# Performance work log

Hardware: AMD Instinct MI355X
Metric: run time of the kernel (lower is better)

## Reference

```python
import jax, jax.numpy as jnp
import numpy as np

# --- fixed module hyperparameters (from init_kwargs) ---
B, N, DIM = 1, 1024, 1024
HEADS, KV_HEADS, DH = 16, 4, 64
BS = 32                 # block_size
NUM_SEL = 8             # num_selected_blocks (< num blocks, so min() is NUM_SEL)
MEM = 1                 # num_compressed_mem_kv
W = N // BS             # num compress blocks (seq divisible by block -> no padding paths)
G = HEADS // KV_HEADS   # grouped queries per kv head
CDIM = BS * DH          # compress mlp input dim
HID = CDIM              # compress_mlp_expand_factor = 1.0
EPS = 1e-6


def setup_inputs() -> dict:
    key = jax.random.key(0)
    ks = jax.random.split(key, 12)
    s = 0.02
    f32 = jnp.float32
    return {
        "inp": jax.random.normal(ks[0], (B, N, DIM), f32),
        "g_norm": jnp.ones((DIM,), f32),                                   # RMSNorm weight
        "w_qkv": jax.random.normal(ks[1], (DIM, (HEADS + 2 * KV_HEADS) * DH), f32) * s,
        "mem_kv": jax.random.normal(ks[2], (2, KV_HEADS, MEM, DH), f32) * s,
        "k_pos": jax.random.normal(ks[3], (KV_HEADS, BS, DH), f32) * s,    # intra-block pos
        "v_pos": jax.random.normal(ks[4], (KV_HEADS, BS, DH), f32) * s,
        "k_w1": jax.random.normal(ks[5], (CDIM, HID), f32) * s,
        "k_b1": jnp.zeros((HID,), f32),
        "k_w2": jax.random.normal(ks[6], (HID, DH), f32) * s,
        "k_b2": jnp.zeros((DH,), f32),
        "v_w1": jax.random.normal(ks[7], (CDIM, HID), f32) * s,
        "v_b1": jnp.zeros((HID,), f32),
        "v_w2": jax.random.normal(ks[8], (HID, DH), f32) * s,
        "v_b2": jnp.zeros((DH,), f32),
        "gate_w": jax.random.normal(ks[9], (DIM, 2 * HEADS), f32) * s,
        "gate_b": jnp.full((2 * HEADS,), -2.0, f32),                       # bias init from source
        "w_out": jax.random.normal(ks[10], (HEADS * DH, DIM), f32) * s,
    }


def _rotary(x):
    # interleaved rotary (rotary-embedding-torch default), x: (b, h, n, d)
    n, d = x.shape[-2], x.shape[-1]
    inv_freq = 1.0 / (10000.0 ** (jnp.arange(0, d, 2, dtype=jnp.float32) / d))
    freqs = jnp.arange(n, dtype=jnp.float32)[:, None] * inv_freq            # (n, d/2)
    cos = jnp.repeat(jnp.cos(freqs), 2, axis=-1).astype(x.dtype)
    sin = jnp.repeat(jnp.sin(freqs), 2, axis=-1).astype(x.dtype)
    xr = jnp.stack([-x[..., 1::2], x[..., 0::2]], axis=-1).reshape(x.shape)  # rotate_half
    return x * cos + xr * sin


def reference(inp, g_norm, w_qkv, mem_kv, k_pos, v_pos,
              k_w1, k_b1, k_w2, k_b2, v_w1, v_b1, v_w2, v_b2,
              gate_w, gate_b, w_out):
    scale = DH ** -0.5
    # RMSNorm
    x = inp * jax.lax.rsqrt(jnp.mean(jnp.square(inp), -1, keepdims=True) + EPS) * g_norm
    qkv = x @ w_qkv
    q = qkv[..., : HEADS * DH].reshape(B, N, HEADS, DH).transpose(0, 2, 1, 3)
    k = qkv[..., HEADS * DH : (HEADS + KV_HEADS) * DH].reshape(B, N, KV_HEADS, DH).transpose(0, 2, 1, 3)
    v = qkv[..., (HEADS + KV_HEADS) * DH :].reshape(B, N, KV_HEADS, DH).transpose(0, 2, 1, 3)

    # --- compressed branch: MLP-pool each block of BS keys/values ---
    kpe = k + jnp.tile(k_pos, (1, W, 1))[None]               # (B,KV,N,DH)
    vpe = v + jnp.tile(v_pos, (1, W, 1))[None]
    ck = jax.nn.relu(kpe.reshape(B, KV_HEADS, W, CDIM) @ k_w1 + k_b1) @ k_w2 + k_b2   # (B,KV,W,DH)
    cv = jax.nn.relu(vpe.reshape(B, KV_HEADS, W, CDIM) @ v_w1 + v_b1) @ v_w2 + v_b2
    ck = jnp.concatenate([jnp.broadcast_to(mem_kv[0], (B, KV_HEADS, MEM, DH)), ck], axis=2)
    cv = jnp.concatenate([jnp.broadcast_to(mem_kv[1], (B, KV_HEADS, MEM, DH)), cv], axis=2)

    qg = q.reshape(B, KV_HEADS, G, N, DH)
    csim = jnp.einsum('bhgid,bhjd->bhgij', qg, ck) * scale   # (B,KV,G,N,MEM+W)
    cattn = jax.nn.softmax(csim, axis=-1)
    c_out = jnp.einsum('bhgij,bhjd->bhgid', cattn, cv).reshape(B, HEADS, N, DH)

    # rotary only for the fine branch (applied after compressed attention)
    q = _rotary(q)
    k = _rotary(k)

    # --- block selection from compressed similarities (query heads share) ---
    imp = csim[..., MEM:].mean(axis=2)                       # (B,KV,N,W)
    imp = jnp.pad(imp, ((0, 0), (0, 0), (0, 0), (1, 0)), constant_values=-1000.0)
    imp = jax.nn.softmax(imp, axis=-1)[..., 1:]
    sel_vals, sel_idx = jax.lax.top_k(imp, NUM_SEL)          # (B,KV,N,S)
    fmask = sel_vals > 1e-10

    # always include each query's own block (diagonal block), fully attended
    own = jnp.broadcast_to((jnp.arange(N) // BS)[None, None, :, None], (B, KV_HEADS, N, 1))
    sel_idx = jnp.concatenate([sel_idx, own], axis=-1)       # (B,KV,N,S+1)
    fmask = jnp.concatenate([fmask, jnp.ones(own.shape, bool)], axis=-1)

    # --- gather selected KV blocks per query position (irregular access) ---
    kb = k.reshape(B, KV_HEADS, W, BS, DH)
    vb = v.reshape(B, KV_HEADS, W, BS, DH)
    b_ix = jnp.arange(B)[:, None, None, None]
    h_ix = jnp.arange(KV_HEADS)[None, :, None, None]
    J = (NUM_SEL + 1) * BS
    fk = kb[b_ix, h_ix, sel_idx].reshape(B, KV_HEADS, N, J, DH)
    fv = vb[b_ix, h_ix, sel_idx].reshape(B, KV_HEADS, N, J, DH)
    fmask = jnp.repeat(fmask, BS, axis=-1)                   # (B,KV,N,J)

    fq = q.reshape(B, KV_HEADS, G, N, DH)
    fsim = jnp.einsum('bhgid,bhijd->bhgij', fq, fk) * scale  # (B,KV,G,N,J)
    fsim = jnp.where(fmask[:, :, None], fsim, -jnp.finfo(fsim.dtype).max)
    fattn = jax.nn.softmax(fsim, axis=-1)
    f_out = jnp.einsum('bhgij,bhijd->bhgid', fattn, fv).reshape(B, HEADS, N, DH)

    # --- learned sigmoid gating of the two branches ---
    gates = jax.nn.sigmoid(x @ gate_w + gate_b).reshape(B, N, HEADS, 2).transpose(0, 2, 1, 3)
    out = gates[..., 0:1] * c_out + gates[..., 1:2] * f_out  # (B,H,N,DH)
    out = out.transpose(0, 2, 1, 3).reshape(B, N, HEADS * DH)
    return out @ w_out
```

## Files before the change

### kernel.cpp

```cpp
#include <hip/hip_runtime.h>
#include <math.h>

#define NTOK 1024
#define DDIM 1024
#define HEADS 16
#define KVH 4
#define DH 64
#define BSZ 32
#define NSEL 8
#define WBLK 32
#define GQ 4
#define CDIM 2048
#define HIDN 2048
#define QKVD 1536
#define SCALE 0.125f
#define NEGINF (-__builtin_inff())

typedef unsigned short u16;
typedef u16   u16x8  __attribute__((ext_vector_type(8)));
typedef short short8 __attribute__((ext_vector_type(8)));
typedef float f32x4  __attribute__((ext_vector_type(4)));

__device__ __forceinline__ u16 f2bf(float f) {
    unsigned u = __float_as_uint(f);
    return (u16)((u + 0x7fffu + ((u >> 16) & 1u)) >> 16);
}
__device__ __forceinline__ float bf2f(u16 h) { return __uint_as_float(((unsigned)h) << 16); }

__device__ __forceinline__ void glds16(const void* g, void* l) {
    __builtin_amdgcn_global_load_lds(
        (const __attribute__((address_space(1))) unsigned int*)g,
        (__attribute__((address_space(3))) unsigned int*)l, 16, 0, 0);
}

__device__ __forceinline__ size_t tiled_off(int row, int k, int K) {
    return ((size_t)((row >> 4) * (K >> 5) + (k >> 5)) * 64 +
            ((row & 15) | (((k >> 3) & 3) << 4))) * 8;
}

__global__ void rmsnorm_kernel(const float* __restrict__ inp, const float* __restrict__ g,
                               u16* __restrict__ xhi, u16* __restrict__ xlo) {
    int t = threadIdx.x;
    int half = t >> 7, tid = t & 127;
    int n = blockIdx.x * 2 + half;
    const float4* row = (const float4*)(inp + (size_t)n * DDIM);
    float4 v0 = row[tid * 2], v1 = row[tid * 2 + 1];
    float ss = v0.x*v0.x + v0.y*v0.y + v0.z*v0.z + v0.w*v0.w
             + v1.x*v1.x + v1.y*v1.y + v1.z*v1.z + v1.w*v1.w;
    for (int off = 32; off; off >>= 1) ss += __shfl_down(ss, off);
    __shared__ float red[4];
    if ((t & 63) == 0) red[t >> 6] = ss;
    __syncthreads();
    float tot = red[half * 2] + red[half * 2 + 1];
    float r = 1.f / sqrtf(tot * (1.f / DDIM) + 1e-6f);
    const float4* gp = (const float4*)g;
    float4 g0 = gp[tid * 2], g1 = gp[tid * 2 + 1];
    float o[8] = { v0.x*r*g0.x, v0.y*r*g0.y, v0.z*r*g0.z, v0.w*r*g0.w,
                   v1.x*r*g1.x, v1.y*r*g1.y, v1.z*r*g1.z, v1.w*r*g1.w };
    u16x8 h, l;
#pragma unroll
    for (int i = 0; i < 8; ++i) {
        u16 hh = f2bf(o[i]);
        h[i] = hh;
        l[i] = f2bf(o[i] - bf2f(hh));
    }
    size_t ob = tiled_off(n, tid * 8, DDIM);
    *(u16x8*)&xhi[ob] = h;
    *(u16x8*)&xlo[ob] = l;
}

__global__ void transpose_split(const float* __restrict__ W, u16* __restrict__ Thi,
                                u16* __restrict__ Tlo, int K, int N) {
    __shared__ float tile[64][65];
    int k0 = blockIdx.y * 64, n0 = blockIdx.x * 64;
    int t = threadIdx.x;
    int r = t >> 4, c4 = (t & 15) * 4;
#pragma unroll
    for (int p = 0; p < 4; ++p) {
        float4 v = *(const float4*)&W[(size_t)(k0 + r + p * 16) * N + n0 + c4];
        tile[r + p * 16][c4 + 0] = v.x;
        tile[r + p * 16][c4 + 1] = v.y;
        tile[r + p * 16][c4 + 2] = v.z;
        tile[r + p * 16][c4 + 3] = v.w;
    }
    __syncthreads();
    int n = t >> 2, ks = (t & 3) * 16;
#pragma unroll
    for (int c = 0; c < 2; ++c) {
        u16x8 h, l;
#pragma unroll
        for (int j = 0; j < 8; ++j) {
            float v = tile[ks + c * 8 + j][n];
            u16 hh = f2bf(v);
            h[j] = hh;
            l[j] = f2bf(v - bf2f(hh));
        }
        size_t ob = tiled_off(n0 + n, k0 + ks + c * 8, K);
        *(u16x8*)&Thi[ob] = h;
        if (Tlo) *(u16x8*)&Tlo[ob] = l;
    }
}

__global__ void pad_small_tiled(const float* __restrict__ W, const float* __restrict__ b,
                                u16* __restrict__ Thi, u16* __restrict__ Tlo,
                                float* __restrict__ bias_pad, int K, int Xn, int KLOG) {
    int idx = blockIdx.x * 256 + threadIdx.x;
    int k = (idx & ((K >> 3) - 1)) * 8;
    int n = idx >> (KLOG - 3);
    if (n >= 128) return;
    u16x8 h, l;
#pragma unroll
    for (int j = 0; j < 8; ++j) {
        float v = (n < Xn) ? W[(size_t)(k + j) * Xn + n] : 0.f;
        u16 hh = f2bf(v);
        h[j] = hh;
        l[j] = f2bf(v - bf2f(hh));
    }
    size_t ob = tiled_off(n, k, K);
    *(u16x8*)&Thi[ob] = h;
    *(u16x8*)&Tlo[ob] = l;
    if (k == 0) bias_pad[n] = (n < Xn) ? b[n] : 0.f;
}

template<int SPLIT, int ACT, int FINAL>
__global__ __launch_bounds__(256, 1)
void gemm_tiled(const u16* __restrict__ Ahi0, const u16* __restrict__ Alo0,
                const u16* __restrict__ Bhi0, const u16* __restrict__ Blo0,
                const float* __restrict__ bias0, float* __restrict__ C0,
                const u16* __restrict__ Ahi1, const u16* __restrict__ Alo1,
                const u16* __restrict__ Bhi1, const u16* __restrict__ Blo1,
                const float* __restrict__ bias1, float* __restrict__ C1,
                int M, int N, int K, int S) {
    int batch = blockIdx.z / S;
    int s = blockIdx.z - batch * S;
    const u16* Ahi = batch ? Ahi1 : Ahi0;
    const u16* Alo = batch ? Alo1 : Alo0;
    const u16* Bhi = batch ? Bhi1 : Bhi0;
    const u16* Blo = batch ? Blo1 : Blo0;
    const float* bias = batch ? bias1 : bias0;
    float* C = batch ? C1 : C0;

    constexpr int PARTS = (SPLIT == 3) ? 2 : 1;
    __shared__ u16 smA[2 * PARTS * 8 * 512];
    __shared__ u16 smB[2 * PARTS * 8 * 512];

    int tid = threadIdx.x;
    int w = tid >> 6, L = tid & 63;
    int m15 = L & 15, q = L >> 4;
    int KT = K >> 5;
    int rowTile = blockIdx.y * 8, colTile = blockIdx.x * 8;
    int NIT = (K / S) >> 5;
    int kb0 = s * NIT;
    int aw = w & 1, bw = w >> 1;

    f32x4 acc[4][4];
#pragma unroll
    for (int i = 0; i < 4; ++i)
#pragma unroll
        for (int j = 0; j < 4; ++j) acc[i][j] = (f32x4){0.f, 0.f, 0.f, 0.f};

    auto stage = [&](int buf, int kb) {
#pragma unroll
        for (int rl = 0; rl < 2; ++rl) {
            int rb = 2 * w + rl;
            glds16(Ahi + ((size_t)(rowTile + rb) * KT + kb) * 512 + (size_t)L * 8,
                   &smA[((buf * PARTS + 0) * 8 + rb) * 512]);
            glds16(Bhi + ((size_t)(colTile + rb) * KT + kb) * 512 + (size_t)L * 8,
                   &smB[((buf * PARTS + 0) * 8 + rb) * 512]);
            if constexpr (SPLIT == 3) {
                glds16(Alo + ((size_t)(rowTile + rb) * KT + kb) * 512 + (size_t)L * 8,
                       &smA[((buf * PARTS + 1) * 8 + rb) * 512]);
                glds16(Blo + ((size_t)(colTile + rb) * KT + kb) * 512 + (size_t)L * 8,
                       &smB[((buf * PARTS + 1) * 8 + rb) * 512]);
            }
        }
    };

    stage(0, kb0);
    for (int it = 0; it < NIT; ++it) {
        __syncthreads();
        if (it + 1 < NIT) stage((it + 1) & 1, kb0 + it + 1);
        int buf = it & 1;
        short8 ah[4], bh[4];
#pragma unroll
        for (int i = 0; i < 4; ++i) {
            ah[i] = *(const short8*)&smA[((buf * PARTS + 0) * 8 + aw * 4 + i) * 512 + L * 8];
            bh[i] = *(const short8*)&smB[((buf * PARTS + 0) * 8 + bw * 4 + i) * 512 + L * 8];
        }
        if constexpr (SPLIT == 3) {
            short8 al[4], bl[4];
#pragma unroll
            for (int i = 0; i < 4; ++i) {
                al[i] = *(const short8*)&smA[((buf * PARTS + 1) * 8 + aw * 4 + i) * 512 + L * 8];
                bl[i] = *(const short8*)&smB[((buf * PARTS + 1) * 8 + bw * 4 + i) * 512 + L * 8];
            }
#pragma unroll
            for (int i = 0; i < 4; ++i)
#pragma unroll
                for (int j = 0; j < 4; ++j) {
                    acc[i][j] = __builtin_amdgcn_mfma_f32_16x16x32_bf16(ah[i], bl[j], acc[i][j], 0, 0, 0);
                    acc[i][j] = __builtin_amdgcn_mfma_f32_16x16x32_bf16(al[i], bh[j], acc[i][j], 0, 0, 0);
                    acc[i][j] = __builtin_amdgcn_mfma_f32_16x16x32_bf16(ah[i], bh[j], acc[i][j], 0, 0, 0);
                }
        } else {
#pragma unroll
            for (int i = 0; i < 4; ++i)
#pragma unroll
                for (int j = 0; j < 4; ++j)
                    acc[i][j] = __builtin_amdgcn_mfma_f32_16x16x32_bf16(ah[i], bh[j], acc[i][j], 0, 0, 0);
        }
    }

    if constexpr (FINAL == 0) C += (size_t)s * M * N;
#pragma unroll
    for (int i = 0; i < 4; ++i) {
        int row = rowTile * 16 + aw * 64 + i * 16 + q * 4;
#pragma unroll
        for (int j = 0; j < 4; ++j) {
            int col = colTile * 16 + bw * 64 + j * 16 + m15;
            float bv = (FINAL && bias) ? bias[col] : 0.f;
#pragma unroll
            for (int r = 0; r < 4; ++r) {
                float v = acc[i][j][r];
                if constexpr (FINAL) {
                    v += bv;
                    if (ACT == 1) v = fmaxf(v, 0.f);
                    if (ACT == 2) v = 1.f / (1.f + expf(-v));
                }
                C[(size_t)(row + r) * N + col] = v;
            }
        }
    }
}

template<int ACT>
__global__ void reduce_f32(const float* __restrict__ P0, const float* __restrict__ bias0,
                           float* __restrict__ C0,
                           const float* __restrict__ P1, const float* __restrict__ bias1,
                           float* __restrict__ C1, int S, int M, int N) {
    const float* P = blockIdx.y ? P1 : P0;
    const float* bias = blockIdx.y ? bias1 : bias0;
    float* C = blockIdx.y ? C1 : C0;
    int idx = blockIdx.x * 256 + threadIdx.x;
    int mn4 = (M * N) >> 2;
    if (idx >= mn4) return;
    f32x4 a = ((const f32x4*)P)[idx];
    for (int s = 1; s < S; ++s) a += ((const f32x4*)P)[(size_t)s * mn4 + idx];
    int col = (idx % (N >> 2)) * 4;
    f32x4 o;
#pragma unroll
    for (int j = 0; j < 4; ++j) {
        float v = a[j] + (bias ? bias[col + j] : 0.f);
        if (ACT == 1) v = fmaxf(v, 0.f);
        if (ACT == 2) v = 1.f / (1.f + expf(-v));
        o[j] = v;
    }
    ((f32x4*)C)[idx] = o;
}

__global__ void reduce_hid(const float* __restrict__ P0, const float* __restrict__ b0,
                           u16* __restrict__ hi0, u16* __restrict__ lo0,
                           const float* __restrict__ P1, const float* __restrict__ b1,
                           u16* __restrict__ hi1, u16* __restrict__ lo1, int S) {
    const float* P = blockIdx.y ? P1 : P0;
    const float* bias = blockIdx.y ? b1 : b0;
    u16* hi = blockIdx.y ? hi1 : hi0;
    u16* lo = blockIdx.y ? lo1 : lo0;
    int idx = blockIdx.x * 256 + threadIdx.x;
    int col = (idx & 255) * 8, rowi = idx >> 8;
    size_t base = ((size_t)rowi * HIDN + col) >> 2;
    f32x4 a0 = ((const f32x4*)P)[base], a1 = ((const f32x4*)P)[base + 1];
    for (int s = 1; s < S; ++s) {
        size_t sb = (size_t)s * (128 * HIDN / 4) + base;
        a0 += ((const f32x4*)P)[sb];
        a1 += ((const f32x4*)P)[sb + 1];
    }
    u16x8 h, l;
#pragma unroll
    for (int j = 0; j < 8; ++j) {
        float v = (j < 4 ? a0[j] : a1[j - 4]) + bias[col + j];
        v = fmaxf(v, 0.f);
        u16 hh = f2bf(v);
        h[j] = hh;
        l[j] = f2bf(v - bf2f(hh));
    }
    size_t ob = tiled_off(rowi, col, HIDN);
    *(u16x8*)&hi[ob] = h;
    *(u16x8*)&lo[ob] = l;
}

__global__ void reduce_ckcv(const float* __restrict__ Pk, const float* __restrict__ Pv,
                            const float* __restrict__ mem_kv,
                            const float* __restrict__ kb2, const float* __restrict__ vb2,
                            float* __restrict__ ck, float* __restrict__ cv, int S) {
    int idx = blockIdx.x * 256 + threadIdx.x;
    if (idx >= KVH * 33 * DH) return;
    int d = idx & 63;
    int j = (idx >> 6) % 33;
    int h = idx / (33 * 64);
    float kvv, vvv;
    if (j == 0) {
        kvv = mem_kv[(0 * KVH + h) * DH + d];
        vvv = mem_kv[(1 * KVH + h) * DH + d];
    } else {
        size_t base = (size_t)(h * WBLK + (j - 1)) * 128 + d;
        float ak = Pk[base], av = Pv[base];
        for (int s = 1; s < S; ++s) {
            ak += Pk[(size_t)s * (128 * 128) + base];
            av += Pv[(size_t)s * (128 * 128) + base];
        }
        kvv = ak + kb2[d];
        vvv = av + vb2[d];
    }
    ck[idx] = kvv;
    cv[idx] = vvv;
}

__global__ void build_cmlp_in(const float* __restrict__ qkv, const float* __restrict__ k_pos,
                              const float* __restrict__ v_pos,
                              u16* __restrict__ ckhi, u16* __restrict__ cklo,
                              u16* __restrict__ cvhi, u16* __restrict__ cvlo) {
    int idx = blockIdx.x * 256 + threadIdx.x;
    int k = (idx & 255) * 8;
    int r = idx >> 8;
    int p = k >> 6, d = k & 63;
    int h = r >> 5, wb = r & 31;
    int nn = wb * BSZ + p;
    const float* kq = qkv + (size_t)nn * QKVD + (HEADS + h) * DH + d;
    const float* vq = qkv + (size_t)nn * QKVD + (HEADS + KVH + h) * DH + d;
    const float* kp = k_pos + (size_t)(h * BSZ + p) * DH + d;
    const float* vp = v_pos + (size_t)(h * BSZ + p) * DH + d;
    u16x8 kh, kl, vh, vl;
#pragma unroll
    for (int j = 0; j < 8; ++j) {
        float kv = kq[j] + kp[j];
        float vv = vq[j] + vp[j];
        u16 a = f2bf(kv), b = f2bf(vv);
        kh[j] = a; kl[j] = f2bf(kv - bf2f(a));
        vh[j] = b; vl[j] = f2bf(vv - bf2f(b));
    }
    size_t ob = tiled_off(r, k, CDIM);
    *(u16x8*)&ckhi[ob] = kh; *(u16x8*)&cklo[ob] = kl;
    *(u16x8*)&cvhi[ob] = vh; *(u16x8*)&cvlo[ob] = vl;
}

__global__ void rotary_kernel(const float* __restrict__ qkv,
                              float* __restrict__ qr, float* __restrict__ kr,
                              float* __restrict__ vr) {
    int idx = blockIdx.x * 256 + threadIdx.x;
    int i = idx & 31;
    int n = (idx >> 5) & 1023;
    int hd = idx >> 15;
    if (hd >= 24) return;
    if (hd >= HEADS + KVH) {
        int h = hd - (HEADS + KVH);
        const float* src = qkv + (size_t)n * QKVD + (HEADS + KVH + h) * DH;
        float* dst = vr + ((size_t)h * NTOK + n) * DH;
        dst[2 * i] = src[2 * i];
        dst[2 * i + 1] = src[2 * i + 1];
        return;
    }
    float inv = powf(10000.f, -(float)i / 32.f);
    float fr = (float)n * inv;
    float c = cosf(fr), s = sinf(fr);
    const float* src; float* dst;
    if (hd < HEADS) { src = qkv + (size_t)n * QKVD + hd * DH;          dst = qr + ((size_t)hd * NTOK + n) * DH; }
    else { int h = hd - HEADS;
           src = qkv + (size_t)n * QKVD + (HEADS + h) * DH;            dst = kr + ((size_t)h * NTOK + n) * DH; }
    float x0 = src[2 * i], x1 = src[2 * i + 1];
    dst[2 * i]     = x0 * c - x1 * s;
    dst[2 * i + 1] = x1 * c + x0 * s;
}

__global__ __launch_bounds__(256)
void cattn_kernel(const float* __restrict__ qkv, const float* __restrict__ ck,
                  const float* __restrict__ cv, float* __restrict__ c_out,
                  int* __restrict__ sel, int* __restrict__ selmask) {
    int h = blockIdx.y;
    int tid = threadIdx.x;
    int w = tid >> 6, lane = tid & 63;
    int grp = lane >> 4, sub = lane & 15;
    int n = blockIdx.x * 4 + w;
    __shared__ float cks[33 * 68];
    __shared__ float cvs[33 * 68];
    __shared__ float sims[16 * 36];

    for (int t4 = tid; t4 < 1056; t4 += 256) {
        int half = (t4 >= 528) ? 1 : 0;
        int u = t4 - half * 528;
        int j = u >> 4, d4 = (u & 15) * 4;
        const float* src = (half ? cv : ck) + (size_t)h * 33 * 64 + j * 64 + d4;
        float* dst = (half ? cvs : cks) + j * 68 + d4;
        *(float4*)dst = *(const float4*)src;
    }
    float qreg[64];
    {
        const float4* qp4 = (const float4*)(qkv + (size_t)n * QKVD + (h * GQ + grp) * DH);
#pragma unroll
        for (int c = 0; c < 16; ++c) {
            float4 v = qp4[c];
            qreg[4 * c] = v.x; qreg[4 * c + 1] = v.y; qreg[4 * c + 2] = v.z; qreg[4 * c + 3] = v.w;
        }
    }
    __syncthreads();

#pragma unroll
    for (int r = 0; r < 3; ++r) {
        int j = r * 16 + sub;
        if (j < 33) {
            float acc = 0.f;
#pragma unroll
            for (int d = 0; d < 64; ++d) acc = fmaf(qreg[d], cks[j * 68 + d], acc);
            sims[(w * 4 + grp) * 36 + j] = acc * SCALE;
        }
    }

    float ival = NEGINF;
    if (lane < 32)
        ival = 0.25f * (sims[(w * 4 + 0) * 36 + 1 + lane] + sims[(w * 4 + 1) * 36 + 1 + lane] +
                        sims[(w * 4 + 2) * 36 + 1 + lane] + sims[(w * 4 + 3) * 36 + 1 + lane]);
    float m = ival;
    for (int off = 32; off; off >>= 1) m = fmaxf(m, __shfl_xor(m, off));
    float e = (lane < 32) ? expf(ival - m) : 0.f;
    float sum = e;
    for (int off = 32; off; off >>= 1) sum += __shfl_xor(sum, off);
    float p = (lane < 32) ? e / sum : NEGINF;

    float v = p;
    int base = (h * NTOK + n) * 9;
    for (int t = 0; t < NSEL; ++t) {
        float bv = v; int bi = lane;
        for (int off = 32; off; off >>= 1) {
            float ov = __shfl_xor(bv, off);
            int   oi = __shfl_xor(bi, off);
            if (ov > bv || (ov == bv && oi < bi)) { bv = ov; bi = oi; }
        }
        if (lane == 0) { sel[base + t] = bi; selmask[base + t] = (bv > 1e-10f) ? 1 : 0; }
        if (lane == bi) v = NEGINF;
    }
    if (lane == 0) { sel[base + NSEL] = n >> 5; selmask[base + NSEL] = 1; }

#pragma unroll
    for (int g = 0; g < 4; ++g) {
        float sv = (lane < 33) ? sims[(w * 4 + g) * 36 + lane] : NEGINF;
        float mm = sv;
        for (int off = 32; off; off >>= 1) mm = fmaxf(mm, __shfl_xor(mm, off));
        float ee = (lane < 33) ? __expf(sv - mm) : 0.f;
        float ssum = ee;
        for (int off = 32; off; off >>= 1) ssum += __shfl_xor(ssum, off);
        if (lane < 33) sims[(w * 4 + g) * 36 + lane] = ee / ssum;
    }

    f32x4 o = (f32x4){0.f, 0.f, 0.f, 0.f};
#pragma unroll
    for (int j = 0; j < 33; ++j) {
        float a = sims[(w * 4 + grp) * 36 + j];
        f32x4 vv = *(const f32x4*)&cvs[j * 68 + sub * 4];
        o += a * vv;
    }
    *(f32x4*)&c_out[(((size_t)(h * GQ + grp)) * NTOK + n) * DH + sub * 4] = o;
}

__global__ void fattn_kernel(const float* __restrict__ qr, const float* __restrict__ kr,
                             const float* __restrict__ vr, const int* __restrict__ sel,
                             const int* __restrict__ selmask, float* __restrict__ f_out) {
    int n = blockIdx.x, h = blockIdx.y;
    int tid = threadIdx.x;
    int w = tid >> 6, lane = tid & 63;
    int grp = lane >> 4, sub = lane & 15;
    __shared__ float qsm[4 * 68];
    __shared__ float Ksm[64 * 64];
    __shared__ float Vsm[64 * 64];
    __shared__ float ps[4 * 68];
    __shared__ float msm[16], lsm[16];
    __shared__ int sel_s[9], msk_s[9];

    if (tid < 9) {
        sel_s[tid] = sel[(h * NTOK + n) * 9 + tid];
        msk_s[tid] = selmask[(h * NTOK + n) * 9 + tid];
    }
    qsm[w * 68 + lane] = qr[(((size_t)(h * GQ + w)) * NTOK + n) * DH + lane];
    f32x4 o4 = (f32x4){0.f, 0.f, 0.f, 0.f};
    float m_run = -3.402823466e38f, l_run = 0.f;
    __syncthreads();

    const float* krh_ = kr + (size_t)h * NTOK * DH;
    const float* vrh_ = vr + (size_t)h * NTOK * DH;

    int rl = lane >> 4, sl = lane & 15;

    auto stageRows = [&](float* dstbuf, const float* src, int bp) {
        int nrow = (bp < 4) ? 64 : 32;
        if (w * 16 < nrow) {
            int myblk = sel_s[bp * 2 + (w >> 1)];
            const float* b_ = src + (size_t)myblk * BSZ * DH;
#pragma unroll
            for (int cc = 0; cc < 4; ++cc) {
                int r = w * 16 + cc * 4 + rl;
                int sg = sl ^ (r & 15);
                glds16(b_ + (size_t)(r & 31) * DH + sg * 4, &dstbuf[(w * 16 + cc * 4) * 64]);
            }
        }
    };

    stageRows(Ksm, krh_, 0);
    stageRows(Vsm, vrh_, 0);

    for (int bp = 0; bp < 5; ++bp) {
        int nrow = (bp < 4) ? 64 : 32;

        asm volatile("s_waitcnt vmcnt(4)" ::: "memory");
        __builtin_amdgcn_sched_barrier(0);

        float s = -3.402823466e38f;
        {
            int jj = w * 16 + sub;
            int b = bp * 2 + (jj >> 5);
            if (jj < nrow && msk_s[b]) {
                int sw = jj & 15;
                const float* Kb = &Ksm[jj * 64];
                f32x4 a0 = (f32x4){0.f, 0.f, 0.f, 0.f};
                f32x4 a1 = (f32x4){0.f, 0.f, 0.f, 0.f};
#pragma unroll
                for (int c = 0; c < 16; c += 2) {
                    f32x4 k4a = *(const f32x4*)&Kb[(c ^ sw) * 4];
                    f32x4 q4a = *(const f32x4*)&qsm[grp * 68 + c * 4];
                    f32x4 k4b = *(const f32x4*)&Kb[((c + 1) ^ sw) * 4];
                    f32x4 q4b = *(const f32x4*)&qsm[grp * 68 + (c + 1) * 4];
                    a0 += q4a * k4a;
                    a1 += q4b * k4b;
                }
                f32x4 at = a0 + a1;
                s = ((at[0] + at[1]) + (at[2] + at[3])) * SCALE;
            }
        }
        float mb = s;
        for (int off = 8; off; off >>= 1) mb = fmaxf(mb, __shfl_xor(mb, off));
        float m_new = fmaxf(m_run, mb);
        float pp = (s > -1e37f) ? __expf(s - m_new) : 0.f;
        float alpha = __expf(m_run - m_new);
        float psum = pp;
        for (int off = 8; off; off >>= 1) psum += __shfl_xor(psum, off);
        l_run = l_run * alpha + psum;
        m_run = m_new;
        ps[w * 68 + grp * 16 + sub] = pp;

        __builtin_amdgcn_sched_barrier(0);
        asm volatile("s_waitcnt lgkmcnt(0)" ::: "memory");
        __builtin_amdgcn_sched_barrier(0);
        if (bp < 4) {
            stageRows(Ksm, krh_, bp + 1);
            asm volatile("s_waitcnt vmcnt(4)" ::: "memory");
        } else {
            asm volatile("s_waitcnt vmcnt(0)" ::: "memory");
        }
        __builtin_amdgcn_sched_barrier(0);

        {
            f32x4 t0 = (f32x4){0.f, 0.f, 0.f, 0.f};
            f32x4 t1 = (f32x4){0.f, 0.f, 0.f, 0.f};
            int jbase = w * 16;
            if (jbase < nrow) {
#pragma unroll
                for (int jq = 0; jq < 4; ++jq) {
                    f32x4 p4 = *(const f32x4*)&ps[w * 68 + grp * 16 + jq * 4];
#pragma unroll
                    for (int r = 0; r < 4; ++r) {
                        int row = jbase + jq * 4 + r;
                        int slot = sub ^ (row & 15);
                        f32x4 vv = *(const f32x4*)&Vsm[row * 64 + slot * 4];
                        if (r & 1) t1 += p4[r] * vv;
                        else       t0 += p4[r] * vv;
                    }
                }
            }
            o4 = o4 * alpha + (t0 + t1);
        }
        if (bp < 4) {
            __builtin_amdgcn_sched_barrier(0);
            asm volatile("s_waitcnt lgkmcnt(0)" ::: "memory");
            __builtin_amdgcn_sched_barrier(0);
            stageRows(Vsm, vrh_, bp + 1);
        }
    }
    if (sub == 0) { msm[w * 4 + grp] = m_run; lsm[w * 4 + grp] = l_run; }
    __syncthreads();
    *(f32x4*)&Ksm[(w * 4 + grp) * 64 + sub * 4] = o4;
    __syncthreads();
    float m0 = msm[0 * 4 + w], m1 = msm[1 * 4 + w], m2 = msm[2 * 4 + w], m3 = msm[3 * 4 + w];
    float M = fmaxf(fmaxf(m0, m1), fmaxf(m2, m3));
    float f0 = __expf(m0 - M), f1 = __expf(m1 - M), f2 = __expf(m2 - M), f3 = __expf(m3 - M);
    float L = lsm[0 * 4 + w] * f0 + lsm[1 * 4 + w] * f1 + lsm[2 * 4 + w] * f2 + lsm[3 * 4 + w] * f3;
    float sum = Ksm[(0 * 4 + w) * 64 + lane] * f0 + Ksm[(1 * 4 + w) * 64 + lane] * f1
              + Ksm[(2 * 4 + w) * 64 + lane] * f2 + Ksm[(3 * 4 + w) * 64 + lane] * f3;
    f_out[(((size_t)(h * GQ + w)) * NTOK + n) * DH + lane] = sum / L;
}

__global__ void mix_kernel(const float* __restrict__ gates, const float* __restrict__ c_out,
                           const float* __restrict__ f_out,
                           u16* __restrict__ mixhi, u16* __restrict__ mixlo) {
    int idx = blockIdx.x * 256 + threadIdx.x;
    int col = (idx & 127) * 8;
    int n = idx >> 7;
    int hd = col >> 6, d = col & 63;
    float g0 = gates[(size_t)n * 128 + hd * 2];
    float g1 = gates[(size_t)n * 128 + hd * 2 + 1];
    size_t hoff = (((size_t)hd) * NTOK + n) * DH + d;
    u16x8 h, l;
#pragma unroll
    for (int j = 0; j < 8; ++j) {
        float v = g0 * c_out[hoff + j] + g1 * f_out[hoff + j];
        u16 hh = f2bf(v);
        h[j] = hh;
        l[j] = f2bf(v - bf2f(hh));
    }
    size_t ob = tiled_off(n, col, DDIM);
    *(u16x8*)&mixhi[ob] = h;
    *(u16x8*)&mixlo[ob] = l;
}

extern "C" void kernel_launch(void* const* d_in, const int* in_sizes, int n_in,
                              void* d_out, int out_size, void* d_ws, size_t ws_size,
                              hipStream_t stream) {
    const float* inp    = (const float*)d_in[0];
    const float* g_norm = (const float*)d_in[1];
    const float* w_qkv  = (const float*)d_in[2];
    const float* mem_kv = (const float*)d_in[3];
    const float* k_pos  = (const float*)d_in[4];
    const float* v_pos  = (const float*)d_in[5];
    const float* k_w1   = (const float*)d_in[6];
    const float* k_b1   = (const float*)d_in[7];
    const float* k_w2   = (const float*)d_in[8];
    const float* k_b2   = (const float*)d_in[9];
    const float* v_w1   = (const float*)d_in[10];
    const float* v_b1   = (const float*)d_in[11];
    const float* v_w2   = (const float*)d_in[12];
    const float* v_b2   = (const float*)d_in[13];
    const float* gate_w = (const float*)d_in[14];
    const float* gate_b = (const float*)d_in[15];
    const float* w_out  = (const float*)d_in[16];
    float* out = (float*)d_out;

    char* wsb = (char*)d_ws;
    size_t off = 0;
    auto alloc = [&](size_t bytes) -> void* {
        void* p = wsb + off;
        off = (off + bytes + 255) & ~(size_t)255;
        return p;
    };
    u16*   xhi    = (u16*)  alloc((size_t)NTOK * DDIM * 2);
    u16*   xlo    = (u16*)  alloc((size_t)NTOK * DDIM * 2);
    float* qkvb   = (float*)alloc((size_t)NTOK * QKVD * 4);
    u16*   wqThi  = (u16*)  alloc((size_t)QKVD * DDIM * 2);
    u16*   wqTlo  = (u16*)  alloc((size_t)QKVD * DDIM * 2);
    u16*   kw1Thi = (u16*)  alloc((size_t)HIDN * CDIM * 2);
    u16*   kw1Tlo = (u16*)  alloc((size_t)HIDN * CDIM * 2);
    u16*   vw1Thi = (u16*)  alloc((size_t)HIDN * CDIM * 2);
    u16*   vw1Tlo = (u16*)  alloc((size_t)HIDN * CDIM * 2);
    u16*   woThi  = (u16*)  alloc((size_t)DDIM * DDIM * 2);
    u16*   gwThi  = (u16*)  alloc((size_t)128 * DDIM * 2);
    u16*   gwTlo  = (u16*)  alloc((size_t)128 * DDIM * 2);
    float* gbp    = (float*)alloc(128 * 4);
    u16*   kw2Thi = (u16*)  alloc((size_t)128 * HIDN * 2);
    u16*   kw2Tlo = (u16*)  alloc((size_t)128 * HIDN * 2);
    float* kb2p   = (float*)alloc(128 * 4);
    u16*   vw2Thi = (u16*)  alloc((size_t)128 * HIDN * 2);
    u16*   vw2Tlo = (u16*)  alloc((size_t)128 * HIDN * 2);
    float* vb2p   = (float*)alloc(128 * 4);
    u16*   cinkhi = (u16*)  alloc((size_t)128 * CDIM * 2);
    u16*   cinklo = (u16*)  alloc((size_t)128 * CDIM * 2);
    u16*   cinvhi = (u16*)  alloc((size_t)128 * CDIM * 2);
    u16*   cinvlo = (u16*)  alloc((size_t)128 * CDIM * 2);
    u16*   hidkhi = (u16*)  alloc((size_t)128 * HIDN * 2);
    u16*   hidklo = (u16*)  alloc((size_t)128 * HIDN * 2);
    u16*   hidvhi = (u16*)  alloc((size_t)128 * HIDN * 2);
    u16*   hidvlo = (u16*)  alloc((size_t)128 * HIDN * 2);
    float* Pg     = (float*)alloc((size_t)8 * NTOK * 128 * 4);
    float* Pm1k   = (float*)alloc((size_t)4 * 128 * HIDN * 4);
    float* Pm1v   = (float*)alloc((size_t)4 * 128 * HIDN * 4);
    float* Pm2k   = (float*)alloc((size_t)8 * 128 * 128 * 4);
    float* Pm2v   = (float*)alloc((size_t)8 * 128 * 128 * 4);
    float* ck     = (float*)alloc((size_t)KVH * 33 * DH * 4);
    float* cv     = (float*)alloc((size_t)KVH * 33 * DH * 4);
    float* qr     = (float*)alloc((size_t)HEADS * NTOK * DH * 4);
    float* kr     = (float*)alloc((size_t)KVH * NTOK * DH * 4);
    float* vr     = (float*)alloc((size_t)KVH * NTOK * DH * 4);
    float* c_out  = (float*)alloc((size_t)HEADS * NTOK * DH * 4);
    float* f_out  = (float*)alloc((size_t)HEADS * NTOK * DH * 4);
    float* gates  = (float*)alloc((size_t)NTOK * 128 * 4);
    int*   sel    = (int*)  alloc((size_t)KVH * NTOK * 9 * 4);
    int*   selmask= (int*)  alloc((size_t)KVH * NTOK * 9 * 4);
    u16*   mixhi  = (u16*)  alloc((size_t)NTOK * DDIM * 2);
    u16*   mixlo  = (u16*)  alloc((size_t)NTOK * DDIM * 2);

    transpose_split<<<dim3(QKVD / 64, DDIM / 64), 256, 0, stream>>>(w_qkv, wqThi, wqTlo, DDIM, QKVD);
    transpose_split<<<dim3(HIDN / 64, CDIM / 64), 256, 0, stream>>>(k_w1, kw1Thi, kw1Tlo, CDIM, HIDN);
    transpose_split<<<dim3(HIDN / 64, CDIM / 64), 256, 0, stream>>>(v_w1, vw1Thi, vw1Tlo, CDIM, HIDN);
    transpose_split<<<dim3(DDIM / 64, DDIM / 64), 256, 0, stream>>>(w_out, woThi, nullptr, DDIM, DDIM);
    pad_small_tiled<<<(128 * DDIM / 8) / 256, 256, 0, stream>>>(gate_w, gate_b, gwThi, gwTlo, gbp, DDIM, 32, 10);
    pad_small_tiled<<<(128 * HIDN / 8) / 256, 256, 0, stream>>>(k_w2, k_b2, kw2Thi, kw2Tlo, kb2p, HIDN, 64, 11);
    pad_small_tiled<<<(128 * HIDN / 8) / 256, 256, 0, stream>>>(v_w2, v_b2, vw2Thi, vw2Tlo, vb2p, HIDN, 64, 11);

    rmsnorm_kernel<<<NTOK / 2, 256, 0, stream>>>(inp, g_norm, xhi, xlo);
    gemm_tiled<3, 0, 1><<<dim3(QKVD / 128, NTOK / 128, 1), 256, 0, stream>>>(
        xhi, xlo, wqThi, wqTlo, nullptr, qkvb,
        xhi, xlo, wqThi, wqTlo, nullptr, qkvb, NTOK, QKVD, DDIM, 1);
    gemm_tiled<3, 0, 0><<<dim3(1, NTOK / 128, 8), 256, 0, stream>>>(
        xhi, xlo, gwThi, gwTlo, nullptr, Pg,
        xhi, xlo, gwThi, gwTlo, nullptr, Pg, NTOK, 128, DDIM, 8);
    reduce_f32<2><<<dim3(128, 1), 256, 0, stream>>>(Pg, gbp, gates, Pg, gbp, gates, 8, NTOK, 128);
    build_cmlp_in<<<128, 256, 0, stream>>>(qkvb, k_pos, v_pos, cinkhi, cinklo, cinvhi, cinvlo);
    gemm_tiled<3, 0, 0><<<dim3(HIDN / 128, 1, 8), 256, 0, stream>>>(
        cinkhi, cinklo, kw1Thi, kw1Tlo, nullptr, Pm1k,
        cinvhi, cinvlo, vw1Thi, vw1Tlo, nullptr, Pm1v, 128, HIDN, CDIM, 4);
    reduce_hid<<<dim3(128, 2), 256, 0, stream>>>(Pm1k, k_b1, hidkhi, hidklo,
                                                 Pm1v, v_b1, hidvhi, hidvlo, 4);
    gemm_tiled<3, 0, 0><<<dim3(1, 1, 16), 256, 0, stream>>>(
        hidkhi, hidklo, kw2Thi, kw2Tlo, nullptr, Pm2k,
        hidvhi, hidvlo, vw2Thi, vw2Tlo, nullptr, Pm2v, 128, 128, HIDN, 8);
    reduce_ckcv<<<33, 256, 0, stream>>>(Pm2k, Pm2v, mem_kv, kb2p, vb2p, ck, cv, 8);
    rotary_kernel<<<(24 * NTOK * 32) / 256, 256, 0, stream>>>(qkvb, qr, kr, vr);
    cattn_kernel<<<dim3(NTOK / 4, KVH), 256, 0, stream>>>(qkvb, ck, cv, c_out, sel, selmask);
    fattn_kernel<<<dim3(NTOK, KVH), 256, 0, stream>>>(qr, kr, vr, sel, selmask, f_out);
    mix_kernel<<<(NTOK * DDIM / 8) / 256, 256, 0, stream>>>(gates, c_out, f_out, mixhi, mixlo);
    gemm_tiled<1, 0, 1><<<dim3(DDIM / 128, NTOK / 128, 1), 256, 0, stream>>>(
        mixhi, mixhi, woThi, woThi, nullptr, out,
        mixhi, mixhi, woThi, woThi, nullptr, out, NTOK, DDIM, DDIM, 1);
}
```

Before: 345.3 us.

## Merge weight-prep and RMSNorm launches into one kernel; vectorize rotary and cattn dot

Folds the four transpose_split launches, three pad_small_tiled launches and the rmsnorm launch into a single prep_kernel that dispatches on blockIdx ranges. This removes seven launch gaps and the tail idle time between small kernels. Separately, the rotary kernel now uses float2 loads and stores with fast __expf/__sincosf intrinsics, and the compressed-attention q·k dot product uses f32x4 vector accumulators with two partial sums. The fast intrinsics and the reordered summation change numerics slightly.

```diff
diff --git a/kernel.cpp b/kernel.cpp
--- a/kernel.cpp
+++ b/kernel.cpp
@@ -38,17 +38,72 @@
             ((row & 15) | (((k >> 3) & 3) << 4))) * 8;
 }
 
-__global__ void rmsnorm_kernel(const float* __restrict__ inp, const float* __restrict__ g,
-                               u16* __restrict__ xhi, u16* __restrict__ xlo) {
+__device__ __forceinline__ void transpose_body(const float* __restrict__ W,
+                                               u16* __restrict__ Thi, u16* __restrict__ Tlo,
+                                               int K, int N, int bx, int by,
+                                               float (*tile)[65]) {
+    int k0 = by * 64, n0 = bx * 64;
+    int t = threadIdx.x;
+    int r = t >> 4, c4 = (t & 15) * 4;
+#pragma unroll
+    for (int p = 0; p < 4; ++p) {
+        float4 v = *(const float4*)&W[(size_t)(k0 + r + p * 16) * N + n0 + c4];
+        tile[r + p * 16][c4 + 0] = v.x;
+        tile[r + p * 16][c4 + 1] = v.y;
+        tile[r + p * 16][c4 + 2] = v.z;
+        tile[r + p * 16][c4 + 3] = v.w;
+    }
+    __syncthreads();
+    int n = t >> 2, ks = (t & 3) * 16;
+#pragma unroll
+    for (int c = 0; c < 2; ++c) {
+        u16x8 h, l;
+#pragma unroll
+        for (int j = 0; j < 8; ++j) {
+            float v = tile[ks + c * 8 + j][n];
+            u16 hh = f2bf(v);
+            h[j] = hh;
+            l[j] = f2bf(v - bf2f(hh));
+        }
+        size_t ob = tiled_off(n0 + n, k0 + ks + c * 8, K);
+        *(u16x8*)&Thi[ob] = h;
+        if (Tlo) *(u16x8*)&Tlo[ob] = l;
+    }
+}
+
+__device__ __forceinline__ void pad_body(const float* __restrict__ W, const float* __restrict__ b,
+                                         u16* __restrict__ Thi, u16* __restrict__ Tlo,
+                                         float* __restrict__ bias_pad, int K, int Xn, int KLOG,
+                                         int bx) {
+    int idx = bx * 256 + threadIdx.x;
+    int k = (idx & ((K >> 3) - 1)) * 8;
+    int n = idx >> (KLOG - 3);
+    if (n >= 128) return;
+    u16x8 h, l;
+#pragma unroll
+    for (int j = 0; j < 8; ++j) {
+        float v = (n < Xn) ? W[(size_t)(k + j) * Xn + n] : 0.f;
+        u16 hh = f2bf(v);
+        h[j] = hh;
+        l[j] = f2bf(v - bf2f(hh));
+    }
+    size_t ob = tiled_off(n, k, K);
+    *(u16x8*)&Thi[ob] = h;
+    *(u16x8*)&Tlo[ob] = l;
+    if (k == 0) bias_pad[n] = (n < Xn) ? b[n] : 0.f;
+}
+
+__device__ __forceinline__ void rms_body(const float* __restrict__ inp, const float* __restrict__ g,
+                                         u16* __restrict__ xhi, u16* __restrict__ xlo,
+                                         int bx, float* red) {
     int t = threadIdx.x;
     int half = t >> 7, tid = t & 127;
-    int n = blockIdx.x * 2 + half;
+    int n = bx * 2 + half;
     const float4* row = (const float4*)(inp + (size_t)n * DDIM);
     float4 v0 = row[tid * 2], v1 = row[tid * 2 + 1];
     float ss = v0.x*v0.x + v0.y*v0.y + v0.z*v0.z + v0.w*v0.w
              + v1.x*v1.x + v1.y*v1.y + v1.z*v1.z + v1.w*v1.w;
     for (int off = 32; off; off >>= 1) ss += __shfl_down(ss, off);
-    __shared__ float red[4];
     if ((t & 63) == 0) red[t >> 6] = ss;
     __syncthreads();
     float tot = red[half * 2] + red[half * 2 + 1];
@@ -69,57 +124,41 @@
     *(u16x8*)&xlo[ob] = l;
 }
 
-__global__ void transpose_split(const float* __restrict__ W, u16* __restrict__ Thi,
-                                u16* __restrict__ Tlo, int K, int N) {
+__global__ void prep_kernel(const float* __restrict__ w_qkv, const float* __restrict__ k_w1,
+                            const float* __restrict__ v_w1, const float* __restrict__ w_out,
+                            const float* __restrict__ gate_w, const float* __restrict__ gate_b,
+                            const float* __restrict__ k_w2, const float* __restrict__ k_b2,
+                            const float* __restrict__ v_w2, const float* __restrict__ v_b2,
+                            const float* __restrict__ inp, const float* __restrict__ g_norm,
+                            u16* wqThi, u16* wqTlo, u16* kw1Thi, u16* kw1Tlo,
+                            u16* vw1Thi, u16* vw1Tlo, u16* woThi,
+                            u16* gwThi, u16* gwTlo, float* gbp,
+                            u16* kw2Thi, u16* kw2Tlo, float* kb2p,
+                            u16* vw2Thi, u16* vw2Tlo, float* vb2p,
+                            u16* xhi, u16* xlo) {
     __shared__ float tile[64][65];
-    int k0 = blockIdx.y * 64, n0 = blockIdx.x * 64;
-    int t = threadIdx.x;
-    int r = t >> 4, c4 = (t & 15) * 4;
-#pragma unroll
-    for (int p = 0; p < 4; ++p) {
-        float4 v = *(const float4*)&W[(size_t)(k0 + r + p * 16) * N + n0 + c4];
-        tile[r + p * 16][c4 + 0] = v.x;
-        tile[r + p * 16][c4 + 1] = v.y;
-        tile[r + p * 16][c4 + 2] = v.z;
-        tile[r + p * 16][c4 + 3] = v.w;
-    }
-    __syncthreads();
-    int n = t >> 2, ks = (t & 3) * 16;
-#pragma unroll
-    for (int c = 0; c < 2; ++c) {
-        u16x8 h, l;
-#pragma unroll
-        for (int j = 0; j < 8; ++j) {
-            float v = tile[ks + c * 8 + j][n];
-            u16 hh = f2bf(v);
-            h[j] = hh;
-            l[j] = f2bf(v - bf2f(hh));
-        }
-        size_t ob = tiled_off(n0 + n, k0 + ks + c * 8, K);
-        *(u16x8*)&Thi[ob] = h;
-        if (Tlo) *(u16x8*)&Tlo[ob] = l;
-    }
-}
-
-__global__ void pad_small_tiled(const float* __restrict__ W, const float* __restrict__ b,
-                                u16* __restrict__ Thi, u16* __restrict__ Tlo,
-                                float* __restrict__ bias_pad, int K, int Xn, int KLOG) {
-    int idx = blockIdx.x * 256 + threadIdx.x;
-    int k = (idx & ((K >> 3) - 1)) * 8;
-    int n = idx >> (KLOG - 3);
-    if (n >= 128) return;
-    u16x8 h, l;
-#pragma unroll
-    for (int j = 0; j < 8; ++j) {
-        float v = (n < Xn) ? W[(size_t)(k + j) * Xn + n] : 0.f;
-        u16 hh = f2bf(v);
-        h[j] = hh;
-        l[j] = f2bf(v - bf2f(hh));
-    }
-    size_t ob = tiled_off(n, k, K);
-    *(u16x8*)&Thi[ob] = h;
-    *(u16x8*)&Tlo[ob] = l;
-    if (k == 0) bias_pad[n] = (n < Xn) ? b[n] : 0.f;
+    __shared__ float red[4];
+    int b = blockIdx.x;
+    if (b < 384) {
+        transpose_body(w_qkv, wqThi, wqTlo, DDIM, QKVD, b % 24, b / 24, tile);
+    } else if (b < 1408) {
+        int r = b - 384;
+        transpose_body(k_w1, kw1Thi, kw1Tlo, CDIM, HIDN, r & 31, r >> 5, tile);
+    } else if (b < 2432) {
+        int r = b - 1408;
+        transpose_body(v_w1, vw1Thi, vw1Tlo, CDIM, HIDN, r & 31, r >> 5, tile);
+    } else if (b < 2688) {
+        int r = b - 2432;
+        transpose_body(w_out, woThi, nullptr, DDIM, DDIM, r & 15, r >> 4, tile);
+    } else if (b < 2752) {
+        pad_body(gate_w, gate_b, gwThi, gwTlo, gbp, DDIM, 32, 10, b - 2688);
+    } else if (b < 2880) {
+        pad_body(k_w2, k_b2, kw2Thi, kw2Tlo, kb2p, HIDN, 64, 11, b - 2752);
+    } else if (b < 3008) {
+        pad_body(v_w2, v_b2, vw2Thi, vw2Tlo, vb2p, HIDN, 64, 11, b - 2880);
+    } else {
+        rms_body(inp, g_norm, xhi, xlo, b - 3008, red);
+    }
 }
 
 template<int SPLIT, int ACT, int FINAL>
@@ -356,20 +395,22 @@
         int h = hd - (HEADS + KVH);
         const float* src = qkv + (size_t)n * QKVD + (HEADS + KVH + h) * DH;
         float* dst = vr + ((size_t)h * NTOK + n) * DH;
-        dst[2 * i] = src[2 * i];
-        dst[2 * i + 1] = src[2 * i + 1];
+        *(float2*)&dst[2 * i] = *(const float2*)&src[2 * i];
         return;
     }
-    float inv = powf(10000.f, -(float)i / 32.f);
+    float inv = __expf((float)i * -0.28782313662425572f);
     float fr = (float)n * inv;
-    float c = cosf(fr), s = sinf(fr);
+    float s, c;
+    __sincosf(fr, &s, &c);
     const float* src; float* dst;
     if (hd < HEADS) { src = qkv + (size_t)n * QKVD + hd * DH;          dst = qr + ((size_t)hd * NTOK + n) * DH; }
     else { int h = hd - HEADS;
            src = qkv + (size_t)n * QKVD + (HEADS + h) * DH;            dst = kr + ((size_t)h * NTOK + n) * DH; }
-    float x0 = src[2 * i], x1 = src[2 * i + 1];
-    dst[2 * i]     = x0 * c - x1 * s;
-    dst[2 * i + 1] = x1 * c + x0 * s;
+    float2 x = *(const float2*)&src[2 * i];
+    float2 o;
+    o.x = x.x * c - x.y * s;
+    o.y = x.y * c + x.x * s;
+    *(float2*)&dst[2 * i] = o;
 }
 
 __global__ __launch_bounds__(256)
@@ -393,13 +434,13 @@
         float* dst = (half ? cvs : cks) + j * 68 + d4;
         *(float4*)dst = *(const float4*)src;
     }
-    float qreg[64];
+    f32x4 qv[16];
     {
         const float4* qp4 = (const float4*)(qkv + (size_t)n * QKVD + (h * GQ + grp) * DH);
 #pragma unroll
         for (int c = 0; c < 16; ++c) {
             float4 v = qp4[c];
-            qreg[4 * c] = v.x; qreg[4 * c + 1] = v.y; qreg[4 * c + 2] = v.z; qreg[4 * c + 3] = v.w;
+            qv[c] = (f32x4){v.x, v.y, v.z, v.w};
         }
     }
     __syncthreads();
@@ -408,10 +449,15 @@
     for (int r = 0; r < 3; ++r) {
         int j = r * 16 + sub;
         if (j < 33) {
-            float acc = 0.f;
-#pragma unroll
-            for (int d = 0; d < 64; ++d) acc = fmaf(qreg[d], cks[j * 68 + d], acc);
-            sims[(w * 4 + grp) * 36 + j] = acc * SCALE;
+            f32x4 a0 = (f32x4){0.f, 0.f, 0.f, 0.f};
+            f32x4 a1 = (f32x4){0.f, 0.f, 0.f, 0.f};
+#pragma unroll
+            for (int c = 0; c < 16; c += 2) {
+                a0 += qv[c]     * (*(const f32x4*)&cks[j * 68 + c * 4]);
+                a1 += qv[c + 1] * (*(const f32x4*)&cks[j * 68 + (c + 1) * 4]);
+            }
+            f32x4 at = a0 + a1;
+            sims[(w * 4 + grp) * 36 + j] = ((at[0] + at[1]) + (at[2] + at[3])) * SCALE;
         }
     }
 
@@ -693,15 +739,13 @@
     u16*   mixhi  = (u16*)  alloc((size_t)NTOK * DDIM * 2);
     u16*   mixlo  = (u16*)  alloc((size_t)NTOK * DDIM * 2);
 
-    transpose_split<<<dim3(QKVD / 64, DDIM / 64), 256, 0, stream>>>(w_qkv, wqThi, wqTlo, DDIM, QKVD);
-    transpose_split<<<dim3(HIDN / 64, CDIM / 64), 256, 0, stream>>>(k_w1, kw1Thi, kw1Tlo, CDIM, HIDN);
-    transpose_split<<<dim3(HIDN / 64, CDIM / 64), 256, 0, stream>>>(v_w1, vw1Thi, vw1Tlo, CDIM, HIDN);
-    transpose_split<<<dim3(DDIM / 64, DDIM / 64), 256, 0, stream>>>(w_out, woThi, nullptr, DDIM, DDIM);
-    pad_small_tiled<<<(128 * DDIM / 8) / 256, 256, 0, stream>>>(gate_w, gate_b, gwThi, gwTlo, gbp, DDIM, 32, 10);
-    pad_small_tiled<<<(128 * HIDN / 8) / 256, 256, 0, stream>>>(k_w2, k_b2, kw2Thi, kw2Tlo, kb2p, HIDN, 64, 11);
-    pad_small_tiled<<<(128 * HIDN / 8) / 256, 256, 0, stream>>>(v_w2, v_b2, vw2Thi, vw2Tlo, vb2p, HIDN, 64, 11);
-
-    rmsnorm_kernel<<<NTOK / 2, 256, 0, stream>>>(inp, g_norm, xhi, xlo);
+    prep_kernel<<<3520, 256, 0, stream>>>(
+        w_qkv, k_w1, v_w1, w_out, gate_w, gate_b, k_w2, k_b2, v_w2, v_b2,
+        inp, g_norm,
+        wqThi, wqTlo, kw1Thi, kw1Tlo, vw1Thi, vw1Tlo, woThi,
+        gwThi, gwTlo, gbp, kw2Thi, kw2Tlo, kb2p, vw2Thi, vw2Tlo, vb2p,
+        xhi, xlo);
+
     gemm_tiled<3, 0, 1><<<dim3(QKVD / 128, NTOK / 128, 1), 256, 0, stream>>>(
         xhi, xlo, wqThi, wqTlo, nullptr, qkvb,
         xhi, xlo, wqThi, wqTlo, nullptr, qkvb, NTOK, QKVD, DDIM, 1);
```

After: 330.0 us. -4.4%, faster.
